# Kernel optimization log

Measured on AMD Instinct MI355X. Metric: run time of the kernel, lower is better.

The kernel has to match this reference:

```python
import jax, jax.numpy as jnp
import numpy as np

NSAMPLE = 32
EPS = 1e-5


def _fps(xyz, npoint):
    # xyz: [B, N, 3] -> indices [B, npoint] (farthest point sampling, start at idx 0)
    B, N, _ = xyz.shape
    def body(i, state):
        idx, dist, far = state
        idx = idx.at[:, i].set(far)
        centroid = jnp.take_along_axis(xyz, far[:, None, None], axis=1)  # [B,1,3]
        d = jnp.sum((xyz - centroid) ** 2, axis=-1)                      # [B,N]
        dist = jnp.minimum(dist, d)
        far = jnp.argmax(dist, axis=-1).astype(jnp.int32)
        return idx, dist, far
    idx0 = jnp.zeros((B, npoint), jnp.int32)
    dist0 = jnp.full((B, N), 1e10, xyz.dtype)
    far0 = jnp.zeros((B,), jnp.int32)
    idx, _, _ = jax.lax.fori_loop(0, npoint, body, (idx0, dist0, far0))
    return idx


def _knn(query, ref, k):
    # query [B,S,3], ref [B,N,3] -> neighbor idx [B,S,k]
    d = (jnp.sum(query * query, -1)[:, :, None]
         - 2.0 * jnp.einsum('bsc,bnc->bsn', query, ref)
         + jnp.sum(ref * ref, -1)[:, None, :])
    _, idx = jax.lax.top_k(-d, k)
    return idx


def _gather(x, idx):
    # x [B,N,C], idx [B,S,K] -> [B,S,K,C]
    B, S, K = idx.shape
    out = jnp.take_along_axis(x, idx.reshape(B, S * K)[..., None], axis=1)
    return out.reshape(B, S, K, x.shape[-1])


def _set_abstraction(xyz, feat, npoint, weights):
    # xyz [B,N,3], feat [B,N,C]
    fidx = _fps(xyz, npoint)
    new_xyz = jnp.take_along_axis(xyz, fidx[..., None], axis=1)        # [B,S,3]
    nidx = _knn(new_xyz, xyz, NSAMPLE)                                 # [B,S,K]
    g_xyz = _gather(xyz, nidx) - new_xyz[:, :, None, :]                # [B,S,K,3]
    g_feat = _gather(feat, nidx)                                       # [B,S,K,C]
    x = jnp.concatenate([g_xyz, g_feat], axis=-1)                      # [B,S,K,3+C]
    for W in weights:  # 1x1 conv == per-point matmul, then InstanceNorm2d (affine=False) + ReLU
        x = jnp.einsum('bskc,cd->bskd', x, W)
        mu = jnp.mean(x, axis=(1, 2), keepdims=True)
        var = jnp.var(x, axis=(1, 2), keepdims=True)
        x = jax.nn.relu((x - mu) * jax.lax.rsqrt(var + EPS))
    new_feat = jnp.max(x, axis=2)                                      # [B,S,Cout]
    return new_xyz, new_feat, fidx


def setup_inputs() -> dict:
    key = jax.random.key(0)
    ks = jax.random.split(key, 8)
    B, N = 4, 16384
    pc = jax.random.normal(ks[0], (B, 3, N), jnp.float32)
    feature = jax.random.normal(ks[1], (B, 3, N), jnp.float32)
    def w(k, cin, cout):
        return jax.random.normal(k, (cin, cout), jnp.float32) / np.sqrt(cin).astype(np.float32)
    return {
        'pc': pc, 'feature': feature,
        'sa1_w1': w(ks[2], 6, 32),  'sa1_w2': w(ks[3], 32, 32), 'sa1_w3': w(ks[4], 32, 32),
        'sa2_w1': w(ks[5], 35, 64), 'sa2_w2': w(ks[6], 64, 64), 'sa2_w3': w(ks[7], 64, 64),
    }


def reference(pc, feature, sa1_w1, sa1_w2, sa1_w3, sa2_w1, sa2_w2, sa2_w3):
    NPOINT = 4096
    xyz = jnp.transpose(pc, (0, 2, 1))       # [B,N,3]
    feat = jnp.transpose(feature, (0, 2, 1))  # [B,N,3]
    xyz1, feat1, fidx1 = _set_abstraction(xyz, feat, NPOINT // 2, [sa1_w1, sa1_w2, sa1_w3])
    xyz2, feat2, fidx2 = _set_abstraction(xyz1, feat1, NPOINT // 4, [sa2_w1, sa2_w2, sa2_w3])
    # match torch channel-first layout on outputs
    pc_l1 = jnp.transpose(xyz1, (0, 2, 1))
    pc_l2 = jnp.transpose(xyz2, (0, 2, 1))
    feat_l2 = jnp.transpose(feat2, (0, 2, 1))  # [B,64,NPOINT//4]
    return (pc, pc_l1, pc_l2, feat_l2, fidx1, fidx2)
```

## Files before the change

### kernel.cpp

```cpp
#include <hip/hip_runtime.h>
#include <math.h>

namespace {

constexpr int BB = 4;
constexpr int N0 = 16384;
constexpr int S1 = 2048;
constexpr int S2 = 1024;

__device__ __forceinline__ float sq3(float x, float y, float z){
  #pragma clang fp contract(off)
  return x*x + y*y + z*z;
}
__device__ __forceinline__ float sqdist(float ax,float ay,float az,float bx,float by,float bz){
  #pragma clang fp contract(off)
  float dx = ax-bx; float dy = ay-by; float dz = az-bz;
  return dx*dx + dy*dy + dz*dz;
}
__device__ __forceinline__ float dot3(float ax,float ay,float az,float bx,float by,float bz){
  #pragma clang fp contract(off)
  return ax*bx + ay*by + az*bz;
}
__device__ __forceinline__ float knndist(float qs, float dot, float rs){
  #pragma clang fp contract(off)
  return (qs - 2.0f*dot) + rs;
}

__global__ __launch_bounds__(256) void k_setup(const float* __restrict__ pc,
                                               const float* __restrict__ feat,
                                               float* __restrict__ out_pc,
                                               float* __restrict__ xyz,
                                               float* __restrict__ fN,
                                               float* __restrict__ rsq0)
{
  int t = blockIdx.x*256 + threadIdx.x;
  if (t < BB*3*N0) out_pc[t] = pc[t];
  if (t < BB*N0){
    int b = t >> 14, n = t & (N0-1);
    const float* p = pc + (size_t)b*3*N0;
    float x = p[n], y = p[N0+n], z = p[2*N0+n];
    float* q = xyz + (size_t)t*3;
    q[0]=x; q[1]=y; q[2]=z;
    rsq0[t] = sq3(x,y,z);
    const float* f = feat + (size_t)b*3*N0;
    float* g = fN + (size_t)t*3;
    g[0]=f[n]; g[1]=f[N0+n]; g[2]=f[2*N0+n];
  }
}

__device__ __forceinline__ void fps_writeout(int b, int i, float cx, float cy, float cz, int far,
                                             float* sxyz, float* srsq, float* pcl, float* fidxf, int NP)
{
  fidxf[(size_t)b*NP + i] = (float)far;
  float* o = sxyz + ((size_t)b*NP + i)*3;
  o[0]=cx; o[1]=cy; o[2]=cz;
  float* pb = pcl + (size_t)b*3*NP;
  pb[i] = cx; pb[NP+i] = cy; pb[2*NP+i] = cz;
  srsq[(size_t)b*NP + i] = sq3(cx,cy,cz);
}

template<int N, int NP, int BS, int PPT>
__global__ __launch_bounds__(BS) void k_fps(const float* __restrict__ pts,
                                            float* __restrict__ sxyz,
                                            float* __restrict__ srsq,
                                            float* __restrict__ pcl,
                                            float* __restrict__ fidxf)
{
  static_assert(N == BS*PPT, "bad fps shape");
  int b = blockIdx.x, t = threadIdx.x;
  const float* P = pts + (size_t)b*N*3;
  float px[PPT], py[PPT], pz[PPT], dist[PPT];
  #pragma unroll
  for (int j=0;j<PPT;j++){
    int g = t + BS*j;
    px[j]=P[g*3]; py[j]=P[g*3+1]; pz[j]=P[g*3+2];
    dist[j]=1e10f;
  }
  __shared__ unsigned s_maxbits;
  __shared__ int      s_win;
  __shared__ float    s_lo;
  float cx = P[0], cy = P[1], cz = P[2];
  if (t == 0){
    s_maxbits = 0u;
    s_win = 0x7FFFFFFF;
    fps_writeout(b, 0, cx, cy, cz, 0, sxyz, srsq, pcl, fidxf, NP);
  }
  __syncthreads();
  for (int i=1;i<NP;i++){
    float vmax = -1.0f;
    #pragma unroll
    for (int j=0;j<PPT;j++){
      float d  = sqdist(px[j],py[j],pz[j],cx,cy,cz);
      float nd = fminf(dist[j], d);
      dist[j]  = nd;
      vmax = fmaxf(vmax, nd);
    }
    #pragma unroll
    for (int off=32; off>0; off>>=1) vmax = fmaxf(vmax, __shfl_down(vmax, off));
    if ((t & 63) == 0) atomicMax(&s_maxbits, __float_as_uint(vmax));
    __syncthreads();
    if (t == 0){
      unsigned mb = s_maxbits;
      float s = sqrtf(__uint_as_float(mb));
      unsigned xb = mb;
      while (xb > 0u && sqrtf(__uint_as_float(xb - 1u)) == s) xb--;
      s_lo = __uint_as_float(xb);
      s_maxbits = 0u;
      s_win = 0x7FFFFFFF;
    }
    __syncthreads();
    float lo = s_lo;
    int li = 0x7FFFFFFF;
    #pragma unroll
    for (int j=PPT-1;j>=0;j--) if (dist[j] >= lo) li = t + BS*j;
    if (li != 0x7FFFFFFF) atomicMin(&s_win, li);
    __syncthreads();
    int far = s_win;
    cx = P[(size_t)far*3]; cy = P[(size_t)far*3+1]; cz = P[(size_t)far*3+2];
    if (t == 0) fps_writeout(b, i, cx, cy, cz, far, sxyz, srsq, pcl, fidxf, NP);
  }
}

template<int NREF, int PPT, int NQ>
__global__ __launch_bounds__(512) void k_knn(const float* __restrict__ qxyz,
                                             const float* __restrict__ qrsq,
                                             const float* __restrict__ rxyz,
                                             const float* __restrict__ rrsq,
                                             int* __restrict__ nidx)
{
  static_assert(NREF == 512*PPT, "bad knn shape");
  int q = blockIdx.x;
  int b = q / NQ;
  int t = threadIdx.x;
  const float* R  = rxyz + (size_t)b*NREF*3;
  const float* RS = rrsq + (size_t)b*NREF;
  float qx = qxyz[(size_t)q*3], qy = qxyz[(size_t)q*3+1], qz = qxyz[(size_t)q*3+2];
  float qs = qrsq[q];
  unsigned u[PPT];
  #pragma unroll
  for (int j=0;j<PPT;j++){
    int g = t + 512*j;
    float rx=R[g*3], ry=R[g*3+1], rz=R[g*3+2];
    float d = knndist(qs, dot3(qx,qy,qz,rx,ry,rz), RS[g]);
    unsigned bu = __float_as_uint(d);
    u[j] = ((int)bu < 0) ? ~bu : (bu | 0x80000000u);
  }
  __shared__ unsigned hist[256];
  __shared__ unsigned s_pref, s_pm, s_want, s_cnteq;
  __shared__ int s_n;
  __shared__ int s_eq[1024];
  __shared__ int s_ne;
  if (t == 0){ s_pref=0u; s_pm=0u; s_want=32u; s_n=0; s_ne=0; }

  for (int shift=24; shift>=0; shift-=8){
    if (t < 256) hist[t] = 0u;
    __syncthreads();
    unsigned pref = s_pref, pm = s_pm;
    #pragma unroll
    for (int j=0;j<PPT;j++){
      if ((u[j] & pm) == pref) atomicAdd(&hist[(u[j]>>shift)&255], 1u);
    }
    __syncthreads();
    if (t < 64){
      unsigned h0=hist[4*t], h1=hist[4*t+1], h2=hist[4*t+2], h3=hist[4*t+3];
      unsigned ssum = h0+h1+h2+h3;
      unsigned inc = ssum;
      #pragma unroll
      for (int off=1; off<64; off<<=1){
        unsigned o = __shfl_up(inc, off);
        if (t >= off) inc += o;
      }
      unsigned exc = inc - ssum;
      unsigned want = s_want;
      if (exc < want && want <= inc){
        unsigned rem = want - exc;
        unsigned bin, below;
        if      (rem <= h0)       { bin=4*t+0; below=exc; }
        else if (rem <= h0+h1)    { bin=4*t+1; below=exc+h0; }
        else if (rem <= h0+h1+h2) { bin=4*t+2; below=exc+h0+h1; }
        else                      { bin=4*t+3; below=exc+h0+h1+h2; }
        s_pref = pref | (bin << shift);
        s_pm   = pm   | (0xFFu << shift);
        s_want = want - below;
        if (shift == 0) s_cnteq = hist[bin];
      }
    }
    __syncthreads();
  }
  unsigned T = s_pref;
  unsigned krem = s_want;
  unsigned cnteq = s_cnteq;
  int* outq = nidx + (size_t)q*32;
  #pragma unroll
  for (int j=0;j<PPT;j++){
    if (u[j] < T){ int p = atomicAdd(&s_n, 1); outq[p] = t + 512*j; }
  }
  __syncthreads();
  if (cnteq == krem){
    #pragma unroll
    for (int j=0;j<PPT;j++){
      if (u[j] == T){ int p = atomicAdd(&s_n, 1); outq[p] = t + 512*j; }
    }
  } else {
    #pragma unroll
    for (int j=0;j<PPT;j++){
      if (u[j] == T){ int p = atomicAdd(&s_ne, 1); if (p < 1024) s_eq[p] = t + 512*j; }
    }
    __syncthreads();
    if (t == 0){
      int ne = s_ne; if (ne > 1024) ne = 1024;
      int p = s_n;
      int take = (int)krem; if (take > ne) take = ne;
      for (int r=0; r<take; r++){
        int mn = 0x7FFFFFFF, mi = -1;
        for (int e=0; e<ne; e++){ if (s_eq[e] < mn){ mn = s_eq[e]; mi = e; } }
        if (mi < 0) break;
        outq[p++] = mn;
        s_eq[mi] = 0x7FFFFFFF;
      }
    }
  }
}

template<int C>
__device__ __forceinline__ void accum_sums(const float* o, int b, float* sums){
  __shared__ float s_sum[C];
  __shared__ float s_ssq[C];
  int t = threadIdx.x;
  if (t < C){ s_sum[t]=0.f; s_ssq[t]=0.f; }
  __syncthreads();
  int lane = t & 63;
  #pragma unroll
  for (int c=0;c<C;c++){
    float v = o[c], v2 = v*v;
    #pragma unroll
    for (int off=32; off>0; off>>=1){ v += __shfl_down(v, off); v2 += __shfl_down(v2, off); }
    if (lane == 0){ atomicAdd(&s_sum[c], v); atomicAdd(&s_ssq[c], v2); }
  }
  __syncthreads();
  if (t < C){
    atomicAdd(&sums[(b*64+t)*2],   s_sum[t]);
    atomicAdd(&sums[(b*64+t)*2+1], s_ssq[t]);
  }
}

__global__ __launch_bounds__(256) void k_sa1_l1(const float* __restrict__ xyz,
                                                const float* __restrict__ fN,
                                                const float* __restrict__ sxyz,
                                                const int* __restrict__ nidx,
                                                const float* __restrict__ W,
                                                float* __restrict__ xout,
                                                float* __restrict__ sums)
{
  __shared__ float sW[192];
  int t = threadIdx.x;
  if (t < 192) sW[t] = W[t];
  int row = blockIdx.x*256 + t;
  int b = row >> 16;
  int sk = row & 65535;
  int s = sk >> 5;
  int nb = nidx[row];
  const float* pr = xyz  + ((size_t)(b*N0 + nb))*3;
  const float* pq = sxyz + ((size_t)(b*S1 + s ))*3;
  const float* pf = fN   + ((size_t)(b*N0 + nb))*3;
  float i0 = pr[0]-pq[0], i1 = pr[1]-pq[1], i2 = pr[2]-pq[2];
  float i3 = pf[0], i4 = pf[1], i5 = pf[2];
  __syncthreads();
  float o[32];
  #pragma unroll
  for (int c=0;c<32;c++){
    float a = i0*sW[c];
    a = fmaf(i1, sW[ 32+c], a);
    a = fmaf(i2, sW[ 64+c], a);
    a = fmaf(i3, sW[ 96+c], a);
    a = fmaf(i4, sW[128+c], a);
    a = fmaf(i5, sW[160+c], a);
    o[c] = a;
    xout[(size_t)c*262144 + row] = a;
  }
  accum_sums<32>(o, b, sums);
}

template<int CIN, int COUT, int LRPB>
__global__ __launch_bounds__(256) void k_sa_mid(const float* __restrict__ xin,
                                                const float* __restrict__ W,
                                                const float* __restrict__ sums_in,
                                                float* __restrict__ xout,
                                                float* __restrict__ sums_out,
                                                int rows_total, float invM)
{
  __shared__ float sW[CIN*COUT];
  __shared__ float s_mu[CIN];
  __shared__ float s_rs[CIN];
  int t = threadIdx.x;
  int row = blockIdx.x*256 + t;
  int bb = (blockIdx.x*256) >> LRPB;
  for (int i=t; i<CIN*COUT; i+=256) sW[i] = W[i];
  if (t < CIN){
    float sm = sums_in[(bb*64+t)*2], sq = sums_in[(bb*64+t)*2+1];
    float mu = sm*invM;
    float var = fmaxf(sq*invM - mu*mu, 0.f);
    s_mu[t] = mu;
    s_rs[t] = 1.0f/sqrtf(var + 1e-5f);
  }
  __syncthreads();
  float o[COUT];
  #pragma unroll
  for (int d=0;d<COUT;d++) o[d] = 0.f;
  #pragma unroll
  for (int c=0;c<CIN;c++){
    float x = xin[(size_t)c*rows_total + row];
    float v = fmaxf((x - s_mu[c])*s_rs[c], 0.f);
    #pragma unroll
    for (int d=0;d<COUT;d++) o[d] = fmaf(v, sW[c*COUT+d], o[d]);
  }
  #pragma unroll
  for (int d=0;d<COUT;d++) xout[(size_t)d*rows_total + row] = o[d];
  accum_sums<COUT>(o, bb, sums_out);
}

__global__ __launch_bounds__(256) void k_sa2_l1(const float* __restrict__ xyz1,
                                                const float* __restrict__ feat1,
                                                const float* __restrict__ xyz2,
                                                const int* __restrict__ nidx,
                                                const float* __restrict__ W,
                                                float* __restrict__ xout,
                                                float* __restrict__ sums)
{
  __shared__ float sW[35*64];
  int t = threadIdx.x;
  for (int i=t; i<35*64; i+=256) sW[i] = W[i];
  int row = blockIdx.x*256 + t;
  int b = row >> 15;
  int sk = row & 32767;
  int s = sk >> 5;
  int nb = nidx[row];
  const float* pr = xyz1 + ((size_t)(b*S1 + nb))*3;
  const float* pq = xyz2 + ((size_t)(b*S2 + s ))*3;
  const float* pf = feat1 + ((size_t)(b*S1 + nb))*32;
  float i0 = pr[0]-pq[0], i1 = pr[1]-pq[1], i2 = pr[2]-pq[2];
  float fv[32];
  #pragma unroll
  for (int c=0;c<32;c++) fv[c] = pf[c];
  __syncthreads();
  float o[64];
  #pragma unroll
  for (int d=0;d<64;d++){
    float a = i0*sW[d];
    a = fmaf(i1, sW[ 64+d], a);
    a = fmaf(i2, sW[128+d], a);
    o[d] = a;
  }
  #pragma unroll
  for (int c=0;c<32;c++){
    float v = fv[c];
    #pragma unroll
    for (int d=0;d<64;d++) o[d] = fmaf(v, sW[(3+c)*64+d], o[d]);
  }
  #pragma unroll
  for (int d=0;d<64;d++) xout[(size_t)d*131072 + row] = o[d];
  accum_sums<64>(o, b, sums);
}

template<int C, int PTSB, int CF>
__global__ __launch_bounds__(256) void k_pool(const float* __restrict__ xin,
                                              const float* __restrict__ sums_in,
                                              float* __restrict__ out,
                                              int rows_total, float invM)
{
  int t = threadIdx.x;
  int c = t & (C-1);
  int pl = t / C;
  int p = blockIdx.x*(256/C) + pl;
  int b = p / PTSB;
  float sm = sums_in[(b*64+c)*2], sq = sums_in[(b*64+c)*2+1];
  float mu = sm*invM;
  float var = fmaxf(sq*invM - mu*mu, 0.f);
  float rs = 1.0f/sqrtf(var + 1e-5f);
  const float* xp = xin + (size_t)c*rows_total + (size_t)p*32;
  float m = -1e30f;
  #pragma unroll
  for (int k=0;k<32;k++) m = fmaxf(m, xp[k]);
  m = fmaxf((m - mu)*rs, 0.0f);
  if (CF) out[((size_t)(b*C + c))*PTSB + (p - b*PTSB)] = m;
  else    out[(size_t)p*C + c] = m;
}

constexpr size_t WS_XYZ   = 0;
constexpr size_t WS_FN    = WS_XYZ   + 196608;
constexpr size_t WS_RSQ0  = WS_FN    + 196608;
constexpr size_t WS_XYZ1  = WS_RSQ0  + 65536;
constexpr size_t WS_RSQ1  = WS_XYZ1  + 24576;
constexpr size_t WS_XYZ2  = WS_RSQ1  + 8192;
constexpr size_t WS_RSQ2  = WS_XYZ2  + 12288;
constexpr size_t WS_FEAT1 = WS_RSQ2  + 4096;
constexpr size_t WS_SUMS  = WS_FEAT1 + 262144;
constexpr size_t WS_BUFA  = WS_SUMS  + 3072;
constexpr size_t WS_BUFB  = WS_BUFA  + 8388608;
constexpr size_t WS_NIDX1 = WS_BUFB  + 8388608;
constexpr size_t WS_NIDX2 = WS_NIDX1 + 262144;

constexpr size_t OUT1 = 196608;
constexpr size_t OUT2 = 221184;
constexpr size_t OUT3 = 233472;
constexpr size_t OUT4 = 495616;
constexpr size_t OUT5 = 503808;

}

extern "C" void kernel_launch(void* const* d_in, const int* in_sizes, int n_in,
                              void* d_out, int out_size, void* d_ws, size_t ws_size,
                              hipStream_t stream)
{
  (void)in_sizes; (void)n_in; (void)out_size; (void)ws_size;
  const float* pc   = (const float*)d_in[0];
  const float* feat = (const float*)d_in[1];
  const float* W1 = (const float*)d_in[2];
  const float* W2 = (const float*)d_in[3];
  const float* W3 = (const float*)d_in[4];
  const float* W4 = (const float*)d_in[5];
  const float* W5 = (const float*)d_in[6];
  const float* W6 = (const float*)d_in[7];
  float* out = (float*)d_out;
  float* ws  = (float*)d_ws;

  float* xyz   = ws + WS_XYZ;
  float* fN    = ws + WS_FN;
  float* rsq0  = ws + WS_RSQ0;
  float* xyz1  = ws + WS_XYZ1;
  float* rsq1  = ws + WS_RSQ1;
  float* xyz2  = ws + WS_XYZ2;
  float* rsq2  = ws + WS_RSQ2;
  float* feat1 = ws + WS_FEAT1;
  float* sums  = ws + WS_SUMS;
  float* bufA  = ws + WS_BUFA;
  float* bufB  = ws + WS_BUFB;
  int* nidx1   = (int*)(ws + WS_NIDX1);
  int* nidx2   = (int*)(ws + WS_NIDX2);

  (void)hipMemsetAsync(sums, 0, 3072*sizeof(float), stream);

  k_setup<<<768, 256, 0, stream>>>(pc, feat, out, xyz, fN, rsq0);

  k_fps<N0, S1, 1024, 16><<<BB, 1024, 0, stream>>>(xyz, xyz1, rsq1, out+OUT1, out+OUT4);
  k_knn<N0, 32, S1><<<BB*S1, 512, 0, stream>>>(xyz1, rsq1, xyz, rsq0, nidx1);
  k_sa1_l1<<<1024, 256, 0, stream>>>(xyz, fN, xyz1, nidx1, W1, bufA, sums);
  k_sa_mid<32,32,16><<<1024, 256, 0, stream>>>(bufA, W2, sums,       bufB, sums+512,  262144, 1.0f/65536.0f);
  k_sa_mid<32,32,16><<<1024, 256, 0, stream>>>(bufB, W3, sums+512,   bufA, sums+1024, 262144, 1.0f/65536.0f);
  k_pool<32, 2048, 0><<<1024, 256, 0, stream>>>(bufA, sums+1024, feat1, 262144, 1.0f/65536.0f);

  k_fps<S1, S2, 256, 8><<<BB, 256, 0, stream>>>(xyz1, xyz2, rsq2, out+OUT2, out+OUT5);
  k_knn<S1, 4, S2><<<BB*S2, 512, 0, stream>>>(xyz2, rsq2, xyz1, rsq1, nidx2);
  k_sa2_l1<<<512, 256, 0, stream>>>(xyz1, feat1, xyz2, nidx2, W4, bufB, sums+1536);
  k_sa_mid<64,64,15><<<512, 256, 0, stream>>>(bufB, W5, sums+1536, bufA, sums+2048, 131072, 1.0f/32768.0f);
  k_sa_mid<64,64,15><<<512, 256, 0, stream>>>(bufA, W6, sums+2048, bufB, sums+2560, 131072, 1.0f/32768.0f);
  k_pool<64, 1024, 1><<<1024, 256, 0, stream>>>(bufB, sums+2560, out+OUT3, 131072, 1.0f/32768.0f);
}
```

Before: 6.335 ms.

## Fuse FPS argmax into single packed 64-bit wave reduction with one barrier

Each FPS iteration now reduces a packed key (sqrt of the max distance in the high bits, the inverted index in the low bits) across each wave with shuffles. The keys go into a double-buffered shared slot array, and every thread reads the per-wave slots after a single barrier. This replaces three barriers and two shared-memory atomic rounds per iteration. The block shapes also change (stage 1 goes to 512 threads with 32 points per thread, stage 2 to 512 threads with 4 points per thread). The tie-breaking now runs per thread against each thread's own max rather than the global max, which relies on the packed sqrt key to keep the same tie semantics and costs more registers per thread.

```diff
diff --git a/kernel.cpp b/kernel.cpp
--- a/kernel.cpp
+++ b/kernel.cpp
@@ -67,7 +67,10 @@
                                             float* __restrict__ fidxf)
 {
   static_assert(N == BS*PPT, "bad fps shape");
+  constexpr int NW = BS/64;
   int b = blockIdx.x, t = threadIdx.x;
+  int lane = t & 63;
+  int wid  = t >> 6;
   const float* P = pts + (size_t)b*N*3;
   float px[PPT], py[PPT], pz[PPT], dist[PPT];
   #pragma unroll
@@ -76,46 +79,43 @@
     px[j]=P[g*3]; py[j]=P[g*3+1]; pz[j]=P[g*3+2];
     dist[j]=1e10f;
   }
-  __shared__ unsigned s_maxbits;
-  __shared__ int      s_win;
-  __shared__ float    s_lo;
+  __shared__ unsigned long long slot[2][NW];
   float cx = P[0], cy = P[1], cz = P[2];
-  if (t == 0){
-    s_maxbits = 0u;
-    s_win = 0x7FFFFFFF;
-    fps_writeout(b, 0, cx, cy, cz, 0, sxyz, srsq, pcl, fidxf, NP);
-  }
-  __syncthreads();
+  if (t == 0) fps_writeout(b, 0, cx, cy, cz, 0, sxyz, srsq, pcl, fidxf, NP);
   for (int i=1;i<NP;i++){
-    float vmax = -1.0f;
+    int par = i & 1;
+    float msq = -1.0f;
     #pragma unroll
     for (int j=0;j<PPT;j++){
       float d  = sqdist(px[j],py[j],pz[j],cx,cy,cz);
       float nd = fminf(dist[j], d);
       dist[j]  = nd;
-      vmax = fmaxf(vmax, nd);
-    }
-    #pragma unroll
-    for (int off=32; off>0; off>>=1) vmax = fmaxf(vmax, __shfl_down(vmax, off));
-    if ((t & 63) == 0) atomicMax(&s_maxbits, __float_as_uint(vmax));
+      msq = fmaxf(msq, nd);
+    }
+    float s = sqrtf(msq);
+    unsigned xb = __float_as_uint(msq);
+    while (xb > 0u && sqrtf(__uint_as_float(xb - 1u)) == s) xb--;
+    float lo = __uint_as_float(xb);
+    int li = 0x7FFFFFFF;
+    #pragma unroll
+    for (int j=PPT-1;j>=0;j--) if (dist[j] >= lo) li = t + BS*j;
+    unsigned long long key = ((unsigned long long)__float_as_uint(s) << 32)
+                           | (unsigned long long)(unsigned)(~li);
+    #pragma unroll
+    for (int off=32; off>0; off>>=1){
+      unsigned long long o = __shfl_xor(key, off);
+      key = (o > key) ? o : key;
+    }
+    if (lane == 0) slot[par][wid] = key;
     __syncthreads();
-    if (t == 0){
-      unsigned mb = s_maxbits;
-      float s = sqrtf(__uint_as_float(mb));
-      unsigned xb = mb;
-      while (xb > 0u && sqrtf(__uint_as_float(xb - 1u)) == s) xb--;
-      s_lo = __uint_as_float(xb);
-      s_maxbits = 0u;
-      s_win = 0x7FFFFFFF;
-    }
-    __syncthreads();
-    float lo = s_lo;
-    int li = 0x7FFFFFFF;
-    #pragma unroll
-    for (int j=PPT-1;j>=0;j--) if (dist[j] >= lo) li = t + BS*j;
-    if (li != 0x7FFFFFFF) atomicMin(&s_win, li);
-    __syncthreads();
-    int far = s_win;
+    unsigned long long best = slot[par][0];
+    #pragma unroll
+    for (int w=1; w<NW; w++){
+      unsigned long long o = slot[par][w];
+      best = (o > best) ? o : best;
+    }
+    int far = (int)(~(unsigned)best);
+    far = __builtin_amdgcn_readfirstlane(far);
     cx = P[(size_t)far*3]; cy = P[(size_t)far*3+1]; cz = P[(size_t)far*3+2];
     if (t == 0) fps_writeout(b, i, cx, cy, cz, far, sxyz, srsq, pcl, fidxf, NP);
   }
@@ -442,14 +442,14 @@
 
   k_setup<<<768, 256, 0, stream>>>(pc, feat, out, xyz, fN, rsq0);
 
-  k_fps<N0, S1, 1024, 16><<<BB, 1024, 0, stream>>>(xyz, xyz1, rsq1, out+OUT1, out+OUT4);
+  k_fps<N0, S1, 512, 32><<<BB, 512, 0, stream>>>(xyz, xyz1, rsq1, out+OUT1, out+OUT4);
   k_knn<N0, 32, S1><<<BB*S1, 512, 0, stream>>>(xyz1, rsq1, xyz, rsq0, nidx1);
   k_sa1_l1<<<1024, 256, 0, stream>>>(xyz, fN, xyz1, nidx1, W1, bufA, sums);
   k_sa_mid<32,32,16><<<1024, 256, 0, stream>>>(bufA, W2, sums,       bufB, sums+512,  262144, 1.0f/65536.0f);
   k_sa_mid<32,32,16><<<1024, 256, 0, stream>>>(bufB, W3, sums+512,   bufA, sums+1024, 262144, 1.0f/65536.0f);
   k_pool<32, 2048, 0><<<1024, 256, 0, stream>>>(bufA, sums+1024, feat1, 262144, 1.0f/65536.0f);
 
-  k_fps<S1, S2, 256, 8><<<BB, 256, 0, stream>>>(xyz1, xyz2, rsq2, out+OUT2, out+OUT5);
+  k_fps<S1, S2, 512, 4><<<BB, 512, 0, stream>>>(xyz1, xyz2, rsq2, out+OUT2, out+OUT5);
   k_knn<S1, 4, S2><<<BB*S2, 512, 0, stream>>>(xyz2, rsq2, xyz1, rsq1, nidx2);
   k_sa2_l1<<<512, 256, 0, stream>>>(xyz1, feat1, xyz2, nidx2, W4, bufB, sums+1536);
   k_sa_mid<64,64,15><<<512, 256, 0, stream>>>(bufB, W5, sums+1536, bufA, sums+2048, 131072, 1.0f/32768.0f);
```

Result: slower. 7.162 ms (+13.1%).
